# Kernel optimization log

Hardware: AMD Instinct MI355X
Metric: run time of the kernel (lower is better)

## Reference

```python
import jax, jax.numpy as jnp
import numpy as np

EPS = 1e-5


def setup_inputs() -> dict:
    key = jax.random.key(0)
    k0, k1, k2, k3 = jax.random.split(key, 4)
    B, C, H, W = 64, 128, 64, 64
    x = jax.random.normal(k0, (B, C, H, W), dtype=jnp.float32)
    w = jax.random.normal(k1, (C, C, 1), dtype=jnp.float32) * 0.05  # conv1d kernel_size=1 weight
    b = jax.random.normal(k2, (C,), dtype=jnp.float32) * 0.05       # conv1d bias
    s = jax.random.normal(k3, (1, C, 1), dtype=jnp.float32)         # learned per-channel gate logits
    offset = jnp.ones((1,), dtype=jnp.float32) * 8.0                 # module inits offset to 8
    return {"x": x, "w": w, "b": b, "s": s, "offset": offset}


def reference(x, w, b, s, offset):
    B, C, H, W = x.shape
    HW = H * W
    # Checkerboard mask: mask[c, l] = (c + l) % 2  (even channel -> [0,1,0,1,...])
    c_idx = jnp.arange(C)
    l_idx = jnp.arange(HW)
    mask = ((c_idx[:, None] + l_idx[None, :]) % 2).astype(x.dtype)  # (C, HW)

    x_flat = x.reshape(B, C, HW)
    x_masked = x_flat * mask                                         # (B, C, HW)
    # 1x1 conv1d: pointwise channel mix + bias
    z = jnp.einsum('oc,bcl->bol', w[:, :, 0], x_masked) + b[None, :, None]
    pool = z.mean(axis=1)                                            # avgpool over channels -> (B, HW)
    g = jax.nn.sigmoid(pool + offset) + EPS                          # (B, HW)
    s_sig = jax.nn.sigmoid(s[0, :, 0]) + EPS                         # (C,)

    attn_mask = (1.0 - mask)[None] * g[:, None, :] + mask[None] * s_sig[None, :, None]  # (B,C,HW)
    out = x * attn_mask.reshape(B, C, H, W)

    logdet = (C // 2) * jnp.sum(jnp.log(g), axis=-1)                 # (B,)
    logdet = logdet + B * jnp.sum(jnp.log(s_sig)[:, None] * mask)    # scalar broadcast over batch
    return out, logdet
```

## Files before the change

### kernel.cpp

```cpp
#include <hip/hip_runtime.h>
#include <hip/hip_bf16.h>
#include <math.h>


#define EPS 1e-5f
#define NC 128
#define NHW 4096
#define NB 64
#define LT 64
#define NLT (NHW / LT)

typedef __attribute__((ext_vector_type(4))) float f4;

__global__ __launch_bounds__(256) void fused_kernel(const float* __restrict__ x,
                                                    const float* __restrict__ w,
                                                    const float* __restrict__ bias,
                                                    const float* __restrict__ s,
                                                    const float* __restrict__ offp,
                                                    float* __restrict__ out,
                                                    float* __restrict__ logdet) {
    __shared__ float  wpart[256];
    __shared__ float4 pp[4][16];
    __shared__ float  ls[4];

    const int tid  = threadIdx.x;
    const int j    = tid & 15;
    const int cg   = tid >> 4;
    const int wave = tid >> 6;
    const int lane = tid & 63;

    const int lt = blockIdx.x;
    const int b  = blockIdx.y;
    const int l0 = lt * LT;

    const size_t base = (size_t)b * (NC * NHW) + (size_t)(cg * 8) * NHW + l0 + j * 4;
    const float* __restrict__ xp = x + base;

    float4 v[8];
#pragma unroll
    for (int k = 0; k < 8; ++k)
        v[k] = *reinterpret_cast<const float4*>(xp + (size_t)k * NHW);

    {
        const int c  = tid & 127;
        const int o0 = (tid >> 7) * 64;
        const float* __restrict__ wp = w + (size_t)o0 * NC + c;
        float a0 = 0.f, a1 = 0.f, a2 = 0.f, a3 = 0.f;
#pragma unroll
        for (int o = 0; o < 64; o += 4) {
            a0 += wp[(o + 0) * NC];
            a1 += wp[(o + 1) * NC];
            a2 += wp[(o + 2) * NC];
            a3 += wp[(o + 3) * NC];
        }
        wpart[tid] = (a0 + a1) + (a2 + a3);
    }

    float ssig[8];
    float bias_part = 0.f;
    float lss       = 0.f;
#pragma unroll
    for (int k = 0; k < 8; ++k) {
        const int c  = cg * 8 + k;
        const float sg = 1.f / (1.f + __expf(-s[c])) + EPS;
        ssig[k] = sg;
        lss += __logf(sg);
        bias_part += bias[c];
    }
    bias_part *= (1.f / NC);

    __syncthreads();

    float4 acc = make_float4(bias_part, bias_part, bias_part, bias_part);
#pragma unroll
    for (int k = 0; k < 8; ++k) {
        const int c  = cg * 8 + k;
        const float wb = (wpart[c] + wpart[NC + c]) * (1.f / NC);
        if (c & 1) { acc.x += wb * v[k].x; acc.z += wb * v[k].z; }
        else       { acc.y += wb * v[k].y; acc.w += wb * v[k].w; }
    }

#pragma unroll
    for (int off = 16; off <= 32; off <<= 1) {
        acc.x += __shfl_xor(acc.x, off);
        acc.y += __shfl_xor(acc.y, off);
        acc.z += __shfl_xor(acc.z, off);
        acc.w += __shfl_xor(acc.w, off);
        lss   += __shfl_xor(lss,   off);
    }
    if (lane < 16) pp[wave][j] = acc;
    if (lane == 0) ls[wave] = lss;
    __syncthreads();

    const float4 p0 = pp[0][j], p1 = pp[1][j], p2 = pp[2][j], p3 = pp[3][j];
    const float off0 = offp[0];
    float4 g;
    g.x = 1.f / (1.f + __expf(-(p0.x + p1.x + p2.x + p3.x + off0))) + EPS;
    g.y = 1.f / (1.f + __expf(-(p0.y + p1.y + p2.y + p3.y + off0))) + EPS;
    g.z = 1.f / (1.f + __expf(-(p0.z + p1.z + p2.z + p3.z + off0))) + EPS;
    g.w = 1.f / (1.f + __expf(-(p0.w + p1.w + p2.w + p3.w + off0))) + EPS;

    if (wave == 0) {
        float slg = (lane < 16)
                  ? (__logf(g.x) + __logf(g.y) + __logf(g.z) + __logf(g.w))
                  : 0.f;
#pragma unroll
        for (int off = 32; off > 0; off >>= 1) slg += __shfl_down(slg, off);
        if (lane == 0) {
            const float S = ls[0] + ls[1] + ls[2] + ls[3];
            atomicAdd(&logdet[b], 64.f * slg + 2048.f * S);
        }
    }

    float* __restrict__ op = out + base;
#pragma unroll
    for (int k = 0; k < 8; ++k) {
        const int c  = cg * 8 + k;
        const float sc = ssig[k];
        f4 o;
        if (c & 1) { o.x = v[k].x * sc;  o.y = v[k].y * g.y;
                     o.z = v[k].z * sc;  o.w = v[k].w * g.w; }
        else       { o.x = v[k].x * g.x; o.y = v[k].y * sc;
                     o.z = v[k].z * g.z; o.w = v[k].w * sc; }
        __builtin_nontemporal_store(o, reinterpret_cast<f4*>(op + (size_t)k * NHW));
    }
}

extern "C" void kernel_launch(void* const* d_in, const int* in_sizes, int n_in,
                              void* d_out, int out_size, void* d_ws, size_t ws_size,
                              hipStream_t stream) {
    const float* x    = (const float*)d_in[0];
    const float* w    = (const float*)d_in[1];
    const float* bias = (const float*)d_in[2];
    const float* s    = (const float*)d_in[3];
    const float* offp = (const float*)d_in[4];

    float* out    = (float*)d_out;
    float* logdet = out + (size_t)NB * NC * NHW;

    hipMemsetAsync(logdet, 0, NB * sizeof(float), stream);

    fused_kernel<<<dim3(NLT, NB), 256, 0, stream>>>(x, w, bias, s, offp, out, logdet);
}
```

Baseline: 61.28 us.

## Hoist weight column sums and gate constants into a single-block prep kernel

Adds a one-block prep kernel that computes the per-channel column sums of w, sigmoid(s), the mean bias and the constant logdet term into workspace. It also initializes logdet there, which replaces the memset. The main kernel then only loads these precomputed values instead of having every one of the 4096 blocks re-reduce the 128x128 weight matrix and recompute sigmoids and logs. This trades redundant per-block work and an extra barrier for an additional serialized kernel launch with a tiny single-block grid.

```diff
diff --git a/kernel.cpp b/kernel.cpp
--- a/kernel.cpp
+++ b/kernel.cpp
@@ -12,16 +12,64 @@
 
 typedef __attribute__((ext_vector_type(4))) float f4;
 
-__global__ __launch_bounds__(256) void fused_kernel(const float* __restrict__ x,
-                                                    const float* __restrict__ w,
-                                                    const float* __restrict__ bias,
-                                                    const float* __restrict__ s,
-                                                    const float* __restrict__ offp,
-                                                    float* __restrict__ out,
-                                                    float* __restrict__ logdet) {
-    __shared__ float  wpart[256];
+
+__global__ __launch_bounds__(256) void prep_kernel(const float* __restrict__ w,
+                                                   const float* __restrict__ bias,
+                                                   const float* __restrict__ s,
+                                                   float* __restrict__ ws,
+                                                   float* __restrict__ logdet) {
+    __shared__ float wpart[256];
+    __shared__ float lred[NC];
+    __shared__ float bred[NC];
+    __shared__ float ldconst;
+
+    const int tid = threadIdx.x;
+    {
+        const int c  = tid & 127;
+        const int o0 = (tid >> 7) * 64;
+        const float* __restrict__ wp = w + (size_t)o0 * NC + c;
+        float a0 = 0.f, a1 = 0.f, a2 = 0.f, a3 = 0.f;
+        float a4 = 0.f, a5 = 0.f, a6 = 0.f, a7 = 0.f;
+#pragma unroll
+        for (int o = 0; o < 64; o += 8) {
+            a0 += wp[(o + 0) * NC];
+            a1 += wp[(o + 1) * NC];
+            a2 += wp[(o + 2) * NC];
+            a3 += wp[(o + 3) * NC];
+            a4 += wp[(o + 4) * NC];
+            a5 += wp[(o + 5) * NC];
+            a6 += wp[(o + 6) * NC];
+            a7 += wp[(o + 7) * NC];
+        }
+        wpart[tid] = (((a0 + a1) + (a2 + a3)) + ((a4 + a5) + (a6 + a7)));
+    }
+    __syncthreads();
+
+    if (tid < NC) {
+        ws[tid] = (wpart[tid] + wpart[NC + tid]) * (1.f / NC);
+        const float ssig = 1.f / (1.f + expf(-s[tid])) + EPS;
+        ws[NC + tid] = ssig;
+        lred[tid] = logf(ssig);
+        bred[tid] = bias[tid];
+    }
+    __syncthreads();
+
+    if (tid == 0) {
+        double sb = 0.0, sl = 0.0;
+        for (int i = 0; i < NC; ++i) { sb += (double)bred[i]; sl += (double)lred[i]; }
+        ws[256] = (float)(sb / NC);
+        ldconst = (float)((double)NB * (double)(NHW / 2) * sl);
+    }
+    __syncthreads();
+    if (tid < NB) logdet[tid] = ldconst;
+}
+
+__global__ __launch_bounds__(256) void main_kernel(const float* __restrict__ x,
+                                                   const float* __restrict__ ws,
+                                                   const float* __restrict__ offp,
+                                                   float* __restrict__ out,
+                                                   float* __restrict__ logdet) {
     __shared__ float4 pp[4][16];
-    __shared__ float  ls[4];
 
     const int tid  = threadIdx.x;
     const int j    = tid & 15;
@@ -41,41 +89,11 @@
     for (int k = 0; k < 8; ++k)
         v[k] = *reinterpret_cast<const float4*>(xp + (size_t)k * NHW);
 
-    {
-        const int c  = tid & 127;
-        const int o0 = (tid >> 7) * 64;
-        const float* __restrict__ wp = w + (size_t)o0 * NC + c;
-        float a0 = 0.f, a1 = 0.f, a2 = 0.f, a3 = 0.f;
-#pragma unroll
-        for (int o = 0; o < 64; o += 4) {
-            a0 += wp[(o + 0) * NC];
-            a1 += wp[(o + 1) * NC];
-            a2 += wp[(o + 2) * NC];
-            a3 += wp[(o + 3) * NC];
-        }
-        wpart[tid] = (a0 + a1) + (a2 + a3);
-    }
-
-    float ssig[8];
-    float bias_part = 0.f;
-    float lss       = 0.f;
+    float4 acc = make_float4(0.f, 0.f, 0.f, 0.f);
 #pragma unroll
     for (int k = 0; k < 8; ++k) {
-        const int c  = cg * 8 + k;
-        const float sg = 1.f / (1.f + __expf(-s[c])) + EPS;
-        ssig[k] = sg;
-        lss += __logf(sg);
-        bias_part += bias[c];
-    }
-    bias_part *= (1.f / NC);
-
-    __syncthreads();
-
-    float4 acc = make_float4(bias_part, bias_part, bias_part, bias_part);
-#pragma unroll
-    for (int k = 0; k < 8; ++k) {
-        const int c  = cg * 8 + k;
-        const float wb = (wpart[c] + wpart[NC + c]) * (1.f / NC);
+        const int c = cg * 8 + k;
+        const float wb = ws[c];
         if (c & 1) { acc.x += wb * v[k].x; acc.z += wb * v[k].z; }
         else       { acc.y += wb * v[k].y; acc.w += wb * v[k].w; }
     }
@@ -86,19 +104,17 @@
         acc.y += __shfl_xor(acc.y, off);
         acc.z += __shfl_xor(acc.z, off);
         acc.w += __shfl_xor(acc.w, off);
-        lss   += __shfl_xor(lss,   off);
     }
     if (lane < 16) pp[wave][j] = acc;
-    if (lane == 0) ls[wave] = lss;
     __syncthreads();
 
     const float4 p0 = pp[0][j], p1 = pp[1][j], p2 = pp[2][j], p3 = pp[3][j];
-    const float off0 = offp[0];
+    const float cst = ws[256] + offp[0];
     float4 g;
-    g.x = 1.f / (1.f + __expf(-(p0.x + p1.x + p2.x + p3.x + off0))) + EPS;
-    g.y = 1.f / (1.f + __expf(-(p0.y + p1.y + p2.y + p3.y + off0))) + EPS;
-    g.z = 1.f / (1.f + __expf(-(p0.z + p1.z + p2.z + p3.z + off0))) + EPS;
-    g.w = 1.f / (1.f + __expf(-(p0.w + p1.w + p2.w + p3.w + off0))) + EPS;
+    g.x = 1.f / (1.f + __expf(-(p0.x + p1.x + p2.x + p3.x + cst))) + EPS;
+    g.y = 1.f / (1.f + __expf(-(p0.y + p1.y + p2.y + p3.y + cst))) + EPS;
+    g.z = 1.f / (1.f + __expf(-(p0.z + p1.z + p2.z + p3.z + cst))) + EPS;
+    g.w = 1.f / (1.f + __expf(-(p0.w + p1.w + p2.w + p3.w + cst))) + EPS;
 
     if (wave == 0) {
         float slg = (lane < 16)
@@ -106,17 +122,15 @@
                   : 0.f;
 #pragma unroll
         for (int off = 32; off > 0; off >>= 1) slg += __shfl_down(slg, off);
-        if (lane == 0) {
-            const float S = ls[0] + ls[1] + ls[2] + ls[3];
-            atomicAdd(&logdet[b], 64.f * slg + 2048.f * S);
-        }
+        if (lane == 0) atomicAdd(&logdet[b], 64.f * slg);
     }
 
+    const float* __restrict__ ssig = ws + NC;
     float* __restrict__ op = out + base;
 #pragma unroll
     for (int k = 0; k < 8; ++k) {
-        const int c  = cg * 8 + k;
-        const float sc = ssig[k];
+        const int c = cg * 8 + k;
+        const float sc = ssig[c];
         f4 o;
         if (c & 1) { o.x = v[k].x * sc;  o.y = v[k].y * g.y;
                      o.z = v[k].z * sc;  o.w = v[k].w * g.w; }
@@ -137,8 +151,8 @@
 
     float* out    = (float*)d_out;
     float* logdet = out + (size_t)NB * NC * NHW;
+    float* ws     = (float*)d_ws;
 
-    hipMemsetAsync(logdet, 0, NB * sizeof(float), stream);
-
-    fused_kernel<<<dim3(NLT, NB), 256, 0, stream>>>(x, w, bias, s, offp, out, logdet);
+    prep_kernel<<<1, 256, 0, stream>>>(w, bias, s, ws, logdet);
+    main_kernel<<<dim3(NLT, NB), 256, 0, stream>>>(x, ws, offp, out, logdet);
 }
```

After: 58.93 us. 1.04x faster.
